# Optimization experiments

Hardware: AMD Instinct MI355X
Metric: run time of the kernel (lower is better)

Reference implementation:

```python
import jax, jax.numpy as jnp
import numpy as np

NEG = -1000.0  # matches the -1000 masking used in the original module


def setup_inputs() -> dict:
    key = jax.random.key(0)
    k0, k1, k2 = jax.random.split(key, 3)
    B, L, T = 512, 512, 32
    S = T + 2  # states: 0 = START, 1..T = tags, T+1 = STOP
    word_tag_value = jax.random.normal(k0, (B, L, T), dtype=jnp.float32)
    # xavier_uniform-style init for the transition matrix, then mask per the original
    a = float(np.sqrt(6.0 / (S + S)))
    translation = jax.random.uniform(k1, (S, S), dtype=jnp.float32, minval=-a, maxval=a)
    translation = translation.at[:, 0].set(NEG)       # nothing transitions into START
    translation = translation.at[S - 1, :].set(NEG)   # nothing transitions out of STOP
    real_tag = jax.random.randint(k2, (B, L), 1, T + 1)  # tags in 1..T
    return {"word_tag_value": word_tag_value, "translation": translation,
            "real_tag": real_tag, "output_loss": 1}


def _score_path(word_tag_value, translation, real_tag, T):
    # sum of emissions at the gold tags (tags 1..T index emission column tag-1)
    emit = jnp.take_along_axis(word_tag_value, (real_tag - 1)[..., None], axis=2)[..., 0]  # [B, L]
    score_emit = emit.sum(axis=1)
    # sum of transitions along the gold path + START/STOP transitions
    score_trans = translation[real_tag[:, :-1], real_tag[:, 1:]].sum(axis=1)
    score_trans = score_trans + translation[0, real_tag[:, 0]] + translation[real_tag[:, -1], T + 1]
    return score_emit + score_trans  # [B]


def _score_total(word_tag_value, translation, T):
    # forward algorithm (logsumexp recursion) over S = T+2 states
    B, L, _ = word_tag_value.shape
    # pad emissions to S states; START/STOP get NEG emission mid-sequence
    obs = jnp.pad(word_tag_value, ((0, 0), (0, 0), (1, 1)), constant_values=NEG)  # [B, L, S]
    # initial alpha: emissions of step 0 at tag states, 0 at START/STOP (as in original)
    alpha0 = jnp.pad(word_tag_value[:, 0, :], ((0, 0), (1, 1)), constant_values=0.0)  # [B, S]

    def step(alpha, obs_t):
        # scores[prev, cur] = alpha[prev] + obs_t[cur] + translation[prev, cur]
        m = alpha[:, :, None] + obs_t[:, None, :] + translation[None, :, :]  # [B, S, S]
        return jax.nn.logsumexp(m, axis=1), None

    alpha_T, _ = jax.lax.scan(step, alpha0, jnp.swapaxes(obs, 0, 1)[1:])  # scan over L-1 steps
    return jax.nn.logsumexp(alpha_T, axis=1)  # [B]


def reference(word_tag_value, translation, real_tag, output_loss):
    T = word_tag_value.shape[-1]
    if output_loss:
        return _score_total(word_tag_value, translation, T) - _score_path(word_tag_value, translation, real_tag, T)
    return None
```

## Files before the change

kernel.cpp:

```cpp
#include <hip/hip_runtime.h>


#define F2  1.4426950408889634f
#define LN2 0.6931471805599453f

__global__ __launch_bounds__(64) void crf_kernel(
    const float* __restrict__ wtv,
    const float* __restrict__ trans,
    const int*   __restrict__ rtag,
    float* __restrict__ out)
{
    __shared__ __align__(16) float tlds[1156];
    __shared__ __align__(16) float alds[64];

    const int b = blockIdx.x;
    const int l = threadIdx.x;
    const int h = l >> 5;
    const int c = l & 31;

    for (int k = l; k < 1156; k += 64) tlds[k] = trans[k];
    __syncthreads();

    float tc[32];
    #pragma unroll
    for (int k = 0; k < 32; ++k) {
        float tv = h ? tlds[(c + 1) * 34 + (k + 1)]
                     : tlds[(k + 1) * 34 + (c + 1)];
        tc[k] = __builtin_exp2f(F2 * tv);
    }
    float accInit = h ? 0.0f : __builtin_exp2f(F2 * tlds[c + 1]);

    const float* wb = wtv + (size_t)b * (512 * 32);
    const int*   tb = rtag + (size_t)b * 512;

    int tagf = tb[l];
    int tagb = tb[448 + l];
    int tag0 = __builtin_amdgcn_readlane(tagf, 0);
    int ptf  = tag0;
    int pcb  = 33;

    float v0    = wb[c];
    float st    = h ? 1.0f : __builtin_exp2f(F2 * v0);
    float pathE = (!h && (c == tag0 - 1)) ? v0 : 0.0f;
    float pathT = h ? 0.0f : tlds[tag0];
    int scaleE  = 0;

    const int rowstride = h ? -32 : 32;
    float vn[8], vc[8], eo[8];
    {
        const float* p = wb + (h ? 511 * 32 : 32) + c;
        #pragma unroll
        for (int j = 0; j < 8; ++j) vn[j] = p[j * rowstride];
    }

    for (int t0 = 1; t0 <= 249; t0 += 8) {
        #pragma unroll
        for (int j = 0; j < 8; ++j) { vc[j] = vn[j]; eo[j] = __builtin_exp2f(F2 * vc[j]); }
        {
            int i8 = t0 + 8;
            int row8 = h ? (512 - i8) : i8;
            const float* p = wb + row8 * 32 + c;
            #pragma unroll
            for (int j = 0; j < 8; ++j) vn[j] = p[j * rowstride];
        }
        #pragma unroll
        for (int j = 0; j < 8; ++j) {
            const int i = t0 + j;
            if ((i & 63) == 0)                 tagf = tb[i + l];
            if (((i & 63) == 1) && (i != 1))   tagb = tb[((512 - i) & ~63) + l];
            int ctf = __builtin_amdgcn_readlane(tagf, i & 63);
            int ctb = __builtin_amdgcn_readlane(tagb, (512 - i) & 63);

            float wval = h ? st * eo[j] : st;
            alds[l] = wval;
            __builtin_amdgcn_wave_barrier();
            const float4* a4 = (const float4*)(alds + (h << 5));
            float a0 = accInit, a1 = 0.0f, a2 = 0.0f, a3 = 0.0f;
            accInit = 0.0f;
            #pragma unroll
            for (int k = 0; k < 8; ++k) {
                float4 x = a4[k];
                a0 += x.x * tc[4 * k + 0];
                a1 += x.y * tc[4 * k + 1];
                a2 += x.z * tc[4 * k + 2];
                a3 += x.w * tc[4 * k + 3];
            }
            __builtin_amdgcn_wave_barrier();
            float s  = (a0 + a1) + (a2 + a3);
            float ns = h ? s : s * eo[j];

            bool doUpd = (i != 256) || (h == 0);
            st = doUpd ? ns : st;

            int myct = h ? ctb : ctf;
            if ((c == myct - 1) && doUpd) pathE += vc[j];
            int af_ = ptf * 34 + ctf;
            int ab_ = ctb * 34 + pcb;
            float tvv = tlds[h ? ab_ : af_];
            pathT += doUpd ? tvv : 0.0f;
            ptf = ctf;
            if (i != 256) pcb = ctb;
        }
        float m = st;
        m = fmaxf(m, __shfl_xor(m, 1));
        m = fmaxf(m, __shfl_xor(m, 2));
        m = fmaxf(m, __shfl_xor(m, 4));
        m = fmaxf(m, __shfl_xor(m, 8));
        m = fmaxf(m, __shfl_xor(m, 16));
        int e = ((__float_as_int(m) >> 23) & 0xff) - 127;
        st *= __int_as_float((127 - e) << 23);
        scaleE += e;
    }

    float bo   = __shfl_xor(st, 32);
    float prod = st * bo;
    prod += __shfl_xor(prod, 1);
    prod += __shfl_xor(prod, 2);
    prod += __shfl_xor(prod, 4);
    prod += __shfl_xor(prod, 8);
    prod += __shfl_xor(prod, 16);
    int scTot = scaleE + __shfl_xor(scaleE, 32);
    float total = ((float)scTot + __builtin_log2f(prod)) * LN2;

    pathE += __shfl_xor(pathE, 1);
    pathE += __shfl_xor(pathE, 2);
    pathE += __shfl_xor(pathE, 4);
    pathE += __shfl_xor(pathE, 8);
    pathE += __shfl_xor(pathE, 16);
    pathE += __shfl_xor(pathE, 32);
    float pT = pathT + __shfl_xor(pathT, 32) + tlds[ptf * 34 + pcb];

    if (l == 0) out[b] = total - (pathE + pT);
}

extern "C" void kernel_launch(void* const* d_in, const int* in_sizes, int n_in,
                              void* d_out, int out_size, void* d_ws, size_t ws_size,
                              hipStream_t stream) {
    const float* wtv   = (const float*)d_in[0];
    const float* trans = (const float*)d_in[1];
    const int*   rtag  = (const int*)d_in[2];
    (void)in_sizes; (void)n_in; (void)d_ws; (void)ws_size; (void)out_size;
    float* out = (float*)d_out;
    crf_kernel<<<512, 64, 0, stream>>>(wtv, trans, rtag, out);
}
```

Measured before the change: 141.9 us.

## Pack two batch sequences per wave with two states per lane

Each 64-lane wave now processes two batch elements, and every lane owns two CRF states instead of one. Forward and backward halves become 16-lane groups. Gold tags are staged once into LDS rather than fetched with readlane. The intent is to halve the grid to 256 blocks so the 256 CUs of an MI355X each run one wave, and to reuse every LDS alpha read for two states. The cost is a longer per-step dependent chain, since each lane now does twice the FMAs and loads float2 emissions, plus higher register pressure.

```diff
diff --git a/kernel.cpp b/kernel.cpp
--- a/kernel.cpp
+++ b/kernel.cpp
@@ -11,115 +11,147 @@
     float* __restrict__ out)
 {
     __shared__ __align__(16) float tlds[1156];
-    __shared__ __align__(16) float alds[64];
+    __shared__ __align__(16) int   ltag[1024];
+    __shared__ __align__(16) float alds[144];
 
-    const int b = blockIdx.x;
-    const int l = threadIdx.x;
-    const int h = l >> 5;
-    const int c = l & 31;
+    const int l  = threadIdx.x;
+    const int q  = l >> 4;
+    const int c4 = l & 15;
+    const int h  = q & 1;
+    const int bp = q >> 1;
+    const int sA = 2 * c4;
+    const int sB = 2 * c4 + 1;
+
+    const int bbase = blockIdx.x * 2;
 
     for (int k = l; k < 1156; k += 64) tlds[k] = trans[k];
+    {
+        const int* rb = rtag + (size_t)bbase * 512;
+        for (int k = l; k < 1024; k += 64) ltag[k] = rb[k];
+    }
     __syncthreads();
 
-    float tc[32];
+    float tcA[32], tcB[32];
     #pragma unroll
     for (int k = 0; k < 32; ++k) {
-        float tv = h ? tlds[(c + 1) * 34 + (k + 1)]
-                     : tlds[(k + 1) * 34 + (c + 1)];
-        tc[k] = __builtin_exp2f(F2 * tv);
+        float tvA = h ? tlds[(sA + 1) * 34 + (k + 1)] : tlds[(k + 1) * 34 + (sA + 1)];
+        float tvB = h ? tlds[(sB + 1) * 34 + (k + 1)] : tlds[(k + 1) * 34 + (sB + 1)];
+        tcA[k] = __builtin_exp2f(F2 * tvA);
+        tcB[k] = __builtin_exp2f(F2 * tvB);
     }
-    float accInit = h ? 0.0f : __builtin_exp2f(F2 * tlds[c + 1]);
+    float aiA = h ? 0.0f : __builtin_exp2f(F2 * tlds[sA + 1]);
+    float aiB = h ? 0.0f : __builtin_exp2f(F2 * tlds[sB + 1]);
 
-    const float* wb = wtv + (size_t)b * (512 * 32);
-    const int*   tb = rtag + (size_t)b * 512;
+    const float* wb  = wtv + (size_t)(bbase + bp) * (512 * 32);
+    const float* wbl = wb + sA;
 
-    int tagf = tb[l];
-    int tagb = tb[448 + l];
-    int tag0 = __builtin_amdgcn_readlane(tagf, 0);
-    int ptf  = tag0;
-    int pcb  = 33;
+    int tag0 = ltag[bp << 9];
 
-    float v0    = wb[c];
-    float st    = h ? 1.0f : __builtin_exp2f(F2 * v0);
-    float pathE = (!h && (c == tag0 - 1)) ? v0 : 0.0f;
-    float pathT = h ? 0.0f : tlds[tag0];
-    int scaleE  = 0;
+    float2 v0 = make_float2(0.0f, 0.0f);
+    if (!h) v0 = *(const float2*)(wbl);
+    float stA = h ? 1.0f : __builtin_exp2f(F2 * v0.x);
+    float stB = h ? 1.0f : __builtin_exp2f(F2 * v0.y);
+    float pathE = 0.0f;
+    if (!h) {
+        if (sA == tag0 - 1) pathE += v0.x;
+        if (sB == tag0 - 1) pathE += v0.y;
+    }
+    float pathT   = h ? 0.0f : tlds[tag0];
+    int   prevtag = h ? 33 : tag0;
+    int   scaleE  = 0;
 
-    const int rowstride = h ? -32 : 32;
-    float vn[8], vc[8], eo[8];
+    const int rs = h ? -16 : 16;
+    float2 vn[8], vc[8], eo[8];
     {
-        const float* p = wb + (h ? 511 * 32 : 32) + c;
+        const float2* p = (const float2*)(wbl + (h ? 511 * 32 : 32));
         #pragma unroll
-        for (int j = 0; j < 8; ++j) vn[j] = p[j * rowstride];
+        for (int j = 0; j < 8; ++j) vn[j] = p[j * rs];
     }
+
+    float*        ach = alds + q * 36;
+    const float4* a4  = (const float4*)ach;
+    float2*       wp  = (float2*)(ach + sA);
 
     for (int t0 = 1; t0 <= 249; t0 += 8) {
         #pragma unroll
-        for (int j = 0; j < 8; ++j) { vc[j] = vn[j]; eo[j] = __builtin_exp2f(F2 * vc[j]); }
+        for (int j = 0; j < 8; ++j) {
+            vc[j] = vn[j];
+            eo[j].x = __builtin_exp2f(F2 * vc[j].x);
+            eo[j].y = __builtin_exp2f(F2 * vc[j].y);
+        }
         {
             int i8 = t0 + 8;
             int row8 = h ? (512 - i8) : i8;
-            const float* p = wb + row8 * 32 + c;
+            const float2* p = (const float2*)(wb + row8 * 32 + sA);
             #pragma unroll
-            for (int j = 0; j < 8; ++j) vn[j] = p[j * rowstride];
+            for (int j = 0; j < 8; ++j) vn[j] = p[j * rs];
+        }
+        int cts[8];
+        #pragma unroll
+        for (int j = 0; j < 8; ++j) {
+            int i = t0 + j;
+            cts[j] = ltag[(bp << 9) + (h ? (512 - i) : i)];
         }
         #pragma unroll
         for (int j = 0; j < 8; ++j) {
             const int i = t0 + j;
-            if ((i & 63) == 0)                 tagf = tb[i + l];
-            if (((i & 63) == 1) && (i != 1))   tagb = tb[((512 - i) & ~63) + l];
-            int ctf = __builtin_amdgcn_readlane(tagf, i & 63);
-            int ctb = __builtin_amdgcn_readlane(tagb, (512 - i) & 63);
 
-            float wval = h ? st * eo[j] : st;
-            alds[l] = wval;
+            float2 wv;
+            wv.x = h ? stA * eo[j].x : stA;
+            wv.y = h ? stB * eo[j].y : stB;
+            *wp = wv;
             __builtin_amdgcn_wave_barrier();
-            const float4* a4 = (const float4*)(alds + (h << 5));
-            float a0 = accInit, a1 = 0.0f, a2 = 0.0f, a3 = 0.0f;
-            accInit = 0.0f;
+            float a0A = aiA, a1A = 0.0f, a2A = 0.0f, a3A = 0.0f;
+            float a0B = aiB, a1B = 0.0f, a2B = 0.0f, a3B = 0.0f;
+            aiA = 0.0f; aiB = 0.0f;
             #pragma unroll
             for (int k = 0; k < 8; ++k) {
                 float4 x = a4[k];
-                a0 += x.x * tc[4 * k + 0];
-                a1 += x.y * tc[4 * k + 1];
-                a2 += x.z * tc[4 * k + 2];
-                a3 += x.w * tc[4 * k + 3];
+                a0A += x.x * tcA[4 * k + 0]; a1A += x.y * tcA[4 * k + 1];
+                a2A += x.z * tcA[4 * k + 2]; a3A += x.w * tcA[4 * k + 3];
+                a0B += x.x * tcB[4 * k + 0]; a1B += x.y * tcB[4 * k + 1];
+                a2B += x.z * tcB[4 * k + 2]; a3B += x.w * tcB[4 * k + 3];
             }
             __builtin_amdgcn_wave_barrier();
-            float s  = (a0 + a1) + (a2 + a3);
-            float ns = h ? s : s * eo[j];
+            float sAv = (a0A + a1A) + (a2A + a3A);
+            float sBv = (a0B + a1B) + (a2B + a3B);
+            float nsA = h ? sAv : sAv * eo[j].x;
+            float nsB = h ? sBv : sBv * eo[j].y;
 
             bool doUpd = (i != 256) || (h == 0);
-            st = doUpd ? ns : st;
+            stA = doUpd ? nsA : stA;
+            stB = doUpd ? nsB : stB;
 
-            int myct = h ? ctb : ctf;
-            if ((c == myct - 1) && doUpd) pathE += vc[j];
-            int af_ = ptf * 34 + ctf;
-            int ab_ = ctb * 34 + pcb;
-            float tvv = tlds[h ? ab_ : af_];
+            int ct = cts[j];
+            if (doUpd) {
+                if (sA == ct - 1) pathE += vc[j].x;
+                if (sB == ct - 1) pathE += vc[j].y;
+            }
+            int idx = h ? (ct * 34 + prevtag)
+                        : (prevtag * 34 + ct);
+            float tvv = tlds[idx];
             pathT += doUpd ? tvv : 0.0f;
-            ptf = ctf;
-            if (i != 256) pcb = ctb;
+            if (!h || (i != 256)) prevtag = ct;
         }
-        float m = st;
+        float m = fmaxf(stA, stB);
         m = fmaxf(m, __shfl_xor(m, 1));
         m = fmaxf(m, __shfl_xor(m, 2));
         m = fmaxf(m, __shfl_xor(m, 4));
         m = fmaxf(m, __shfl_xor(m, 8));
-        m = fmaxf(m, __shfl_xor(m, 16));
         int e = ((__float_as_int(m) >> 23) & 0xff) - 127;
-        st *= __int_as_float((127 - e) << 23);
+        float sc = __int_as_float((127 - e) << 23);
+        stA *= sc; stB *= sc;
         scaleE += e;
     }
 
-    float bo   = __shfl_xor(st, 32);
-    float prod = st * bo;
+    float boA = __shfl_xor(stA, 16);
+    float boB = __shfl_xor(stB, 16);
+    float prod = stA * boA + stB * boB;
     prod += __shfl_xor(prod, 1);
     prod += __shfl_xor(prod, 2);
     prod += __shfl_xor(prod, 4);
     prod += __shfl_xor(prod, 8);
-    prod += __shfl_xor(prod, 16);
-    int scTot = scaleE + __shfl_xor(scaleE, 32);
+    int scTot = scaleE + __shfl_xor(scaleE, 16);
     float total = ((float)scTot + __builtin_log2f(prod)) * LN2;
 
     pathE += __shfl_xor(pathE, 1);
@@ -127,10 +159,10 @@
     pathE += __shfl_xor(pathE, 4);
     pathE += __shfl_xor(pathE, 8);
     pathE += __shfl_xor(pathE, 16);
-    pathE += __shfl_xor(pathE, 32);
-    float pT = pathT + __shfl_xor(pathT, 32) + tlds[ptf * 34 + pcb];
+    int otag = __shfl_xor(prevtag, 16);
+    float pT = pathT + __shfl_xor(pathT, 16) + tlds[prevtag * 34 + otag];
 
-    if (l == 0) out[b] = total - (pathE + pT);
+    if (!h && c4 == 0) out[bbase + bp] = total - (pathE + pT);
 }
 
 extern "C" void kernel_launch(void* const* d_in, const int* in_sizes, int n_in,
@@ -141,5 +173,5 @@
     const int*   rtag  = (const int*)d_in[2];
     (void)in_sizes; (void)n_in; (void)d_ws; (void)ws_size; (void)out_size;
     float* out = (float*)d_out;
-    crf_kernel<<<512, 64, 0, stream>>>(wtv, trans, rtag, out);
+    crf_kernel<<<256, 64, 0, stream>>>(wtv, trans, rtag, out);
 }
```

Measured after the change: 188.4 us. 32.8% more time.

## Process two batch rows per wave with interleaved forward/backward chains

Applied to the files above, without the earlier changes.

Each 64-lane block now handles two sequences, one per half-wave, and every lane runs both the forward and backward linear-space recursions. The two dependent chains are interleaved so their LDS round-trips and FMAs overlap. Transition exponentials are pre-scaled by a constant bias, which lets renormalisation run every 16 steps instead of every 8; the bias is added back as a fixed exponent count. The gold-path score moves out of the serial loop into a parallel gather at the end, with tags staged in LDS. The grid halves to 256 blocks, and the extra registers for two transition tables may reduce occupancy.

```diff
diff --git a/kernel.cpp b/kernel.cpp
--- a/kernel.cpp
+++ b/kernel.cpp
@@ -1,8 +1,10 @@
 #include <hip/hip_runtime.h>
 
 
-#define F2  1.4426950408889634f
-#define LN2 0.6931471805599453f
+#define F2   1.4426950408889634f
+#define LN2  0.6931471805599453f
+#define BIAS 0.0078125f
+#define BIASCNT 3577
 
 __global__ __launch_bounds__(64) void crf_kernel(
     const float* __restrict__ wtv,
@@ -11,126 +13,171 @@
     float* __restrict__ out)
 {
     __shared__ __align__(16) float tlds[1156];
-    __shared__ __align__(16) float alds[64];
+    __shared__ __align__(16) int   ltag[1024];
+    __shared__ __align__(16) float alds[160];
 
-    const int b = blockIdx.x;
     const int l = threadIdx.x;
-    const int h = l >> 5;
+    const int q = l >> 5;
     const int c = l & 31;
+    const int bbase = blockIdx.x * 2;
 
     for (int k = l; k < 1156; k += 64) tlds[k] = trans[k];
+    {
+        const int* rtb = rtag + (size_t)bbase * 512;
+        for (int k = l; k < 1024; k += 64) ltag[k] = rtb[k];
+    }
     __syncthreads();
 
-    float tc[32];
+    float tcF[32], tcB[32];
     #pragma unroll
     for (int k = 0; k < 32; ++k) {
-        float tv = h ? tlds[(c + 1) * 34 + (k + 1)]
-                     : tlds[(k + 1) * 34 + (c + 1)];
-        tc[k] = __builtin_exp2f(F2 * tv);
+        tcF[k] = __builtin_exp2f(F2 * tlds[(k + 1) * 34 + (c + 1)]) * BIAS;
+        tcB[k] = __builtin_exp2f(F2 * tlds[(c + 1) * 34 + (k + 1)]) * BIAS;
     }
-    float accInit = h ? 0.0f : __builtin_exp2f(F2 * tlds[c + 1]);
+    float aiF = __builtin_exp2f(F2 * tlds[c + 1]) * BIAS;
 
-    const float* wb = wtv + (size_t)b * (512 * 32);
-    const int*   tb = rtag + (size_t)b * 512;
+    const float* wbq = wtv + (size_t)(bbase + q) * (512 * 32);
 
-    int tagf = tb[l];
-    int tagb = tb[448 + l];
-    int tag0 = __builtin_amdgcn_readlane(tagf, 0);
-    int ptf  = tag0;
-    int pcb  = 33;
+    float stF = __builtin_exp2f(F2 * wbq[c]);
+    float stB = 1.0f;
+    int scF = 0, scB = 0;
 
-    float v0    = wb[c];
-    float st    = h ? 1.0f : __builtin_exp2f(F2 * v0);
-    float pathE = (!h && (c == tag0 - 1)) ? v0 : 0.0f;
-    float pathT = h ? 0.0f : tlds[tag0];
-    int scaleE  = 0;
+    float vnF[8], vnB[8], eoF[8], eoB[8];
+    #pragma unroll
+    for (int j = 0; j < 8; ++j) {
+        vnF[j] = wbq[(1 + j) * 32 + c];
+        vnB[j] = wbq[(511 - j) * 32 + c];
+    }
 
-    const int rowstride = h ? -32 : 32;
-    float vn[8], vc[8], eo[8];
-    {
-        const float* p = wb + (h ? 511 * 32 : 32) + c;
-        #pragma unroll
-        for (int j = 0; j < 8; ++j) vn[j] = p[j * rowstride];
-    }
+    float* aF = alds + q * 36;
+    float* aB = alds + 80 + q * 36;
+    const float4* f4 = (const float4*)aF;
+    const float4* b4 = (const float4*)aB;
+
+    float4 ra[8], rb[8];
+
+    aF[c] = stF;
+    __builtin_amdgcn_wave_barrier();
+    #pragma unroll
+    for (int k = 0; k < 8; ++k) ra[k] = f4[k];
+    __builtin_amdgcn_wave_barrier();
 
     for (int t0 = 1; t0 <= 249; t0 += 8) {
         #pragma unroll
-        for (int j = 0; j < 8; ++j) { vc[j] = vn[j]; eo[j] = __builtin_exp2f(F2 * vc[j]); }
+        for (int j = 0; j < 8; ++j) {
+            eoF[j] = __builtin_exp2f(F2 * vnF[j]);
+            eoB[j] = __builtin_exp2f(F2 * vnB[j]);
+        }
         {
-            int i8 = t0 + 8;
-            int row8 = h ? (512 - i8) : i8;
-            const float* p = wb + row8 * 32 + c;
+            const int i8 = t0 + 8;
             #pragma unroll
-            for (int j = 0; j < 8; ++j) vn[j] = p[j * rowstride];
+            for (int j = 0; j < 8; ++j) {
+                vnF[j] = wbq[(i8 + j) * 32 + c];
+                vnB[j] = wbq[(512 - i8 - j) * 32 + c];
+            }
         }
+        const bool resc = ((t0 + 7) & 15) == 0;
         #pragma unroll
         for (int j = 0; j < 8; ++j) {
             const int i = t0 + j;
-            if ((i & 63) == 0)                 tagf = tb[i + l];
-            if (((i & 63) == 1) && (i != 1))   tagb = tb[((512 - i) & ~63) + l];
-            int ctf = __builtin_amdgcn_readlane(tagf, i & 63);
-            int ctb = __builtin_amdgcn_readlane(tagb, (512 - i) & 63);
 
-            float wval = h ? st * eo[j] : st;
-            alds[l] = wval;
+            aB[c] = stB * eoB[j];
             __builtin_amdgcn_wave_barrier();
-            const float4* a4 = (const float4*)(alds + (h << 5));
-            float a0 = accInit, a1 = 0.0f, a2 = 0.0f, a3 = 0.0f;
-            accInit = 0.0f;
             #pragma unroll
-            for (int k = 0; k < 8; ++k) {
-                float4 x = a4[k];
-                a0 += x.x * tc[4 * k + 0];
-                a1 += x.y * tc[4 * k + 1];
-                a2 += x.z * tc[4 * k + 2];
-                a3 += x.w * tc[4 * k + 3];
+            for (int k = 0; k < 8; ++k) rb[k] = b4[k];
+            __builtin_amdgcn_wave_barrier();
+            {
+                float a0 = aiF, a1 = 0.0f, a2 = 0.0f, a3 = 0.0f;
+                aiF = 0.0f;
+                #pragma unroll
+                for (int k = 0; k < 8; ++k) {
+                    float4 x = ra[k];
+                    a0 += x.x * tcF[4 * k + 0]; a1 += x.y * tcF[4 * k + 1];
+                    a2 += x.z * tcF[4 * k + 2]; a3 += x.w * tcF[4 * k + 3];
+                }
+                float s = (a0 + a1) + (a2 + a3);
+                stF = s * eoF[j];
             }
+            if (j == 7 && resc) {
+                float m = stF;
+                m = fmaxf(m, __shfl_xor(m, 1));
+                m = fmaxf(m, __shfl_xor(m, 2));
+                m = fmaxf(m, __shfl_xor(m, 4));
+                m = fmaxf(m, __shfl_xor(m, 8));
+                m = fmaxf(m, __shfl_xor(m, 16));
+                int e = ((__float_as_int(m) >> 23) & 0xff) - 127;
+                stF *= __int_as_float((127 - e) << 23);
+                scF += e;
+            }
+
+            aF[c] = stF;
             __builtin_amdgcn_wave_barrier();
-            float s  = (a0 + a1) + (a2 + a3);
-            float ns = h ? s : s * eo[j];
-
-            bool doUpd = (i != 256) || (h == 0);
-            st = doUpd ? ns : st;
-
-            int myct = h ? ctb : ctf;
-            if ((c == myct - 1) && doUpd) pathE += vc[j];
-            int af_ = ptf * 34 + ctf;
-            int ab_ = ctb * 34 + pcb;
-            float tvv = tlds[h ? ab_ : af_];
-            pathT += doUpd ? tvv : 0.0f;
-            ptf = ctf;
-            if (i != 256) pcb = ctb;
+            #pragma unroll
+            for (int k = 0; k < 8; ++k) ra[k] = f4[k];
+            __builtin_amdgcn_wave_barrier();
+            {
+                float a0 = 0.0f, a1 = 0.0f, a2 = 0.0f, a3 = 0.0f;
+                #pragma unroll
+                for (int k = 0; k < 8; ++k) {
+                    float4 x = rb[k];
+                    a0 += x.x * tcB[4 * k + 0]; a1 += x.y * tcB[4 * k + 1];
+                    a2 += x.z * tcB[4 * k + 2]; a3 += x.w * tcB[4 * k + 3];
+                }
+                float s = (a0 + a1) + (a2 + a3);
+                stB = (i != 256) ? s : stB;
+            }
         }
-        float m = st;
-        m = fmaxf(m, __shfl_xor(m, 1));
-        m = fmaxf(m, __shfl_xor(m, 2));
-        m = fmaxf(m, __shfl_xor(m, 4));
-        m = fmaxf(m, __shfl_xor(m, 8));
-        m = fmaxf(m, __shfl_xor(m, 16));
-        int e = ((__float_as_int(m) >> 23) & 0xff) - 127;
-        st *= __int_as_float((127 - e) << 23);
-        scaleE += e;
+        if (resc) {
+            float m = stB;
+            m = fmaxf(m, __shfl_xor(m, 1));
+            m = fmaxf(m, __shfl_xor(m, 2));
+            m = fmaxf(m, __shfl_xor(m, 4));
+            m = fmaxf(m, __shfl_xor(m, 8));
+            m = fmaxf(m, __shfl_xor(m, 16));
+            int e = ((__float_as_int(m) >> 23) & 0xff) - 127;
+            stB *= __int_as_float((127 - e) << 23);
+            scB += e;
+        }
     }
 
-    float bo   = __shfl_xor(st, 32);
-    float prod = st * bo;
+    float prod = stF * stB;
     prod += __shfl_xor(prod, 1);
     prod += __shfl_xor(prod, 2);
     prod += __shfl_xor(prod, 4);
     prod += __shfl_xor(prod, 8);
     prod += __shfl_xor(prod, 16);
-    int scTot = scaleE + __shfl_xor(scaleE, 32);
-    float total = ((float)scTot + __builtin_log2f(prod)) * LN2;
+    float total = ((float)(scF + scB + BIASCNT) + __builtin_log2f(prod)) * LN2;
 
-    pathE += __shfl_xor(pathE, 1);
-    pathE += __shfl_xor(pathE, 2);
-    pathE += __shfl_xor(pathE, 4);
-    pathE += __shfl_xor(pathE, 8);
-    pathE += __shfl_xor(pathE, 16);
-    pathE += __shfl_xor(pathE, 32);
-    float pT = pathT + __shfl_xor(pathT, 32) + tlds[ptf * 34 + pcb];
-
-    if (l == 0) out[b] = total - (pathE + pT);
+    float ps0 = 0.0f, ps1 = 0.0f;
+    #pragma unroll
+    for (int bb = 0; bb < 2; ++bb) {
+        const float* w  = wtv + (size_t)(bbase + bb) * (512 * 32);
+        const int*   tg = ltag + (bb << 9);
+        int   tcur[8];
+        float em[8];
+        #pragma unroll
+        for (int k = 0; k < 8; ++k) tcur[k] = tg[l + 64 * k];
+        #pragma unroll
+        for (int k = 0; k < 8; ++k) em[k] = w[(l + 64 * k) * 32 + (tcur[k] - 1)];
+        float acc = 0.0f;
+        #pragma unroll
+        for (int k = 0; k < 8; ++k) {
+            int t  = l + 64 * k;
+            int nx = tg[(t + 1) & 511];
+            nx = (t == 511) ? 33 : nx;
+            acc += em[k] + tlds[tcur[k] * 34 + nx];
+        }
+        if (l == 0) acc += tlds[tg[0]];
+        acc += __shfl_xor(acc, 1);
+        acc += __shfl_xor(acc, 2);
+        acc += __shfl_xor(acc, 4);
+        acc += __shfl_xor(acc, 8);
+        acc += __shfl_xor(acc, 16);
+        acc += __shfl_xor(acc, 32);
+        if (bb == 0) ps0 = acc; else ps1 = acc;
+    }
+    float ps = (q == 0) ? ps0 : ps1;
+    if (c == 0) out[bbase + q] = total - ps;
 }
 
 extern "C" void kernel_launch(void* const* d_in, const int* in_sizes, int n_in,
@@ -141,5 +188,5 @@
     const int*   rtag  = (const int*)d_in[2];
     (void)in_sizes; (void)n_in; (void)d_ws; (void)ws_size; (void)out_size;
     float* out = (float*)d_out;
-    crf_kernel<<<512, 64, 0, stream>>>(wtv, trans, rtag, out);
+    crf_kernel<<<256, 64, 0, stream>>>(wtv, trans, rtag, out);
 }
```

Measured after the change: 144.9 us. 2.1% more time.
